# Kernel optimization log

Hardware: AMD Instinct MI355X
Metric: run time of the kernel (lower is better)

## Reference

```python
import jax, jax.numpy as jnp
import numpy as np
from jax import lax
from jax.scipy.special import logsumexp

B, T, K = 256, 1024, 64


def setup_inputs() -> dict:
    key = jax.random.key(0)
    k1, k2, k3 = jax.random.split(key, 3)
    y_true = jax.random.randint(k1, (B, T), 0, K)  # 0 == pad tag
    emissions = jax.random.normal(k2, (B, T, K), dtype=jnp.float32)
    transition = jax.random.normal(k3, (K, K), dtype=jnp.float32) * 0.1
    return {"y_true": y_true, "emissions": emissions, "transition": transition}


def _log_partition(emissions, mask, transition):
    # alpha_0 = emissions[:, 0, :] (TF code does not mask step 0)
    alpha0 = emissions[:, 0, :]  # [B, K]

    def step(alpha, xs):
        emit_t, m_t = xs  # [B, K], [B]
        # score[b, i, j] = alpha[b, i] + transition[i, j] + emit_t[b, j]
        score = alpha[:, :, None] + transition[None, :, :] + emit_t[:, None, :]
        new_a = logsumexp(score, axis=1)  # [B, K]
        new_a = jnp.where(m_t[:, None] > 0, new_a, alpha)
        return new_a, None

    xs = (jnp.swapaxes(emissions[:, 1:, :], 0, 1),  # [T-1, B, K]
          jnp.swapaxes(mask[:, 1:], 0, 1))           # [T-1, B]
    alpha, _ = lax.scan(step, alpha0, xs)
    return logsumexp(alpha, axis=1)  # [B]


def reference(y_true, emissions, transition):
    mask = (y_true != 0).astype(emissions.dtype)  # [B, T]
    yt = y_true.astype(jnp.int32)

    # emission scores of the gold path on masked emissions
    em_masked = emissions * mask[:, :, None]
    e_scores = jnp.take_along_axis(em_masked, yt[:, :, None], axis=2)[..., 0].sum(axis=1)  # [B]

    # transition scores of the gold path
    prev, nxt = yt[:, :-1], yt[:, 1:]
    t_scores = (transition[prev, nxt] * mask[:, 1:]).sum(axis=1)  # [B]

    log_z = _log_partition(emissions, mask, transition)  # [B]
    ll = e_scores + t_scores - log_z
    return -jnp.mean(ll)
```

## Files before the change

### kernel.cpp

```cpp
#include <hip/hip_runtime.h>

#define LOG2E 1.44269504088896340736f
#define LN2   0.69314718055994530942f

typedef short bf8 __attribute__((ext_vector_type(8)));
typedef float f4  __attribute__((ext_vector_type(4)));

static __device__ __forceinline__ unsigned short f2bf_rne(float f) {
    unsigned u = __float_as_uint(f);
    u += 0x7FFFu + ((u >> 16) & 1u);
    return (unsigned short)(u >> 16);
}
static __device__ __forceinline__ unsigned pack_bf_trunc(float lo, float hi) {
    return __builtin_amdgcn_perm(__float_as_uint(hi), __float_as_uint(lo), 0x07060302u);
}

__global__ __attribute__((amdgpu_flat_work_group_size(64, 64), amdgpu_waves_per_eu(1, 4)))
void crf_scan(const int* __restrict__ yg, const float* __restrict__ em,
              const float* __restrict__ tr, unsigned short* __restrict__ Pg)
{
    constexpr int T = 1024, STR = 72;
    const int c = blockIdx.x, b = blockIdx.y;
    const int lane = threadIdx.x, nl = lane & 15, q = lane >> 4;

    __shared__ __align__(16) unsigned short p_sh[64 * STR];
    __shared__ float d_sh[64];

    #pragma unroll
    for (int r = 0; r < 9; ++r) {
        uint4 z; z.x = z.y = z.z = z.w = 0u;
        *(uint4*)&p_sh[lane * STR + r * 8] = z;
    }
    p_sh[lane * STR + lane] = 0x3F80;

    bf8 afr[4][2];
    #pragma unroll
    for (int mt = 0; mt < 4; ++mt)
        #pragma unroll
        for (int kt = 0; kt < 2; ++kt) {
            bf8 v;
            #pragma unroll
            for (int j = 0; j < 8; ++j) {
                const int k = 32 * kt + 8 * q + j, m = 16 * mt + nl;
                v[j] = (short)f2bf_rne(exp2f(tr[k * 64 + m] * LOG2E));
            }
            afr[mt][kt] = v;
        }

    const int t0 = 1 + 64 * c;
    const int nsteps = (c == 15) ? 63 : 64;
    const float* emb = em + (size_t)b * T * 64;

    int tl = t0 + lane; if (tl > T - 1) tl = T - 1;
    const int yvl = yg[b * T + tl];
    const unsigned long long msk = __ballot(lane < nsteps && yvl != 0);

    float ldc = emb[t0 * 64 + lane];
    for (int s = 0; s < nsteps; ++s) {
        int tn = t0 + s + 1; if (tn > T - 1) tn = T - 1;
        const float ldn = emb[tn * 64 + lane];
        if ((msk >> s) & 1ull) {
            d_sh[lane] = exp2f(ldc * LOG2E - 7.0f);
            bf8 bfr[2][4];
            #pragma unroll
            for (int kt = 0; kt < 2; ++kt)
                #pragma unroll
                for (int nt = 0; nt < 4; ++nt)
                    bfr[kt][nt] = *(const bf8*)&p_sh[(16 * nt + nl) * STR + 32 * kt + 8 * q];
            float d16[4][4];
            #pragma unroll
            for (int mt = 0; mt < 4; ++mt)
                #pragma unroll
                for (int r = 0; r < 4; ++r)
                    d16[mt][r] = d_sh[16 * mt + 4 * q + r];
            #pragma unroll
            for (int mt = 0; mt < 4; ++mt)
                #pragma unroll
                for (int nt = 0; nt < 4; ++nt) {
                    f4 acc = __builtin_amdgcn_mfma_f32_16x16x32_bf16(
                                 afr[mt][0], bfr[0][nt], (f4)(0.0f), 0, 0, 0);
                    acc = __builtin_amdgcn_mfma_f32_16x16x32_bf16(
                                 afr[mt][1], bfr[1][nt], acc, 0, 0, 0);
                    const unsigned p0 = pack_bf_trunc(acc[0] * d16[mt][0], acc[1] * d16[mt][1]);
                    const unsigned p1 = pack_bf_trunc(acc[2] * d16[mt][2], acc[3] * d16[mt][3]);
                    uint2 w; w.x = p0; w.y = p1;
                    *(uint2*)&p_sh[(16 * nt + nl) * STR + 16 * mt + 4 * q] = w;
                }
        }
        ldc = ldn;
    }

    unsigned short* pg = Pg + ((size_t)(b * 16 + c) << 12);
    #pragma unroll
    for (int r = 0; r < 8; ++r)
        *(uint4*)(pg + lane * 64 + r * 8) = *(const uint4*)&p_sh[lane * STR + r * 8];
}

__global__ __attribute__((amdgpu_flat_work_group_size(64, 64), amdgpu_waves_per_eu(1, 1)))
void crf_combine(const int* __restrict__ yg, const float* __restrict__ em,
                 const float* __restrict__ tr, const unsigned short* __restrict__ Pg,
                 float* __restrict__ out)
{
    constexpr int T = 1024;
    const int b = blockIdx.x, j = threadIdx.x;
    __shared__ __align__(16) float v_sh[64];

    const float e0 = em[(size_t)b * T * 64 + j];
    float M0 = e0;
    #pragma unroll
    for (int o = 32; o > 0; o >>= 1) M0 = fmaxf(M0, __shfl_xor(M0, o, 64));
    float v = exp2f((e0 - M0) * LOG2E);
    float L = M0;

    const int* yb = yg + b * T;
    int cnt = 0; float ep = 0.f, tp = 0.f;
    for (int t = 1 + j; t < T; t += 64) {
        const int yt = yb[t];
        if (yt != 0) {
            ++cnt;
            tp += tr[yb[t - 1] * 64 + yt];
            ep += em[((size_t)b * T + t) * 64 + yt];
        }
    }
    if (j == 0) {
        const int y0 = yb[0];
        if (y0 != 0) ep += em[(size_t)b * T * 64 + y0];
    }

    const unsigned short* pgb = Pg + ((size_t)(b * 16) << 12);
    for (int c = 0; c < 16; ++c) {
        v_sh[j] = v;
        const unsigned short* row = pgb + ((size_t)c << 12) + j * 64;
        float s0 = 0.f, s1 = 0.f, s2 = 0.f, s3 = 0.f;
        #pragma unroll
        for (int r = 0; r < 8; ++r) {
            const uint4 qq = *(const uint4*)(row + r * 8);
            const float* vp = &v_sh[r * 8];
            s0 = fmaf(__uint_as_float(qq.x << 16),         vp[0], s0);
            s1 = fmaf(__uint_as_float(qq.x & 0xFFFF0000u), vp[1], s1);
            s2 = fmaf(__uint_as_float(qq.y << 16),         vp[2], s2);
            s3 = fmaf(__uint_as_float(qq.y & 0xFFFF0000u), vp[3], s3);
            s0 = fmaf(__uint_as_float(qq.z << 16),         vp[4], s0);
            s1 = fmaf(__uint_as_float(qq.z & 0xFFFF0000u), vp[5], s1);
            s2 = fmaf(__uint_as_float(qq.w << 16),         vp[6], s2);
            s3 = fmaf(__uint_as_float(qq.w & 0xFFFF0000u), vp[7], s3);
        }
        float s = (s0 + s1) + (s2 + s3);
        const unsigned sb = (unsigned)__builtin_amdgcn_readlane((int)__float_as_uint(s), 0);
        const int ef = (int)((sb >> 23) & 0xFF);
        if (ef > 0 && ef < 255 && ef != 127) {
            const int E = ef - 127;
            s *= __uint_as_float((unsigned)(127 - E) << 23);
            L += (float)E * LN2;
        }
        v = s;
    }

    float vs = v, eps = ep, tps = tp; int cs = cnt;
    #pragma unroll
    for (int o = 32; o > 0; o >>= 1) {
        vs  += __shfl_xor(vs, o, 64);
        eps += __shfl_xor(eps, o, 64);
        tps += __shfl_xor(tps, o, 64);
        cs  += __shfl_xor(cs, o, 64);
    }
    if (j == 0) {
        const float logz = L + 7.0f * LN2 * (float)cs + __log2f(vs) * LN2;
        const float ll = eps + tps - logz;
        atomicAdd(out, ll * (-1.0f / 256.0f));
    }
}

extern "C" void kernel_launch(void* const* d_in, const int* in_sizes, int n_in,
                              void* d_out, int out_size, void* d_ws, size_t ws_size,
                              hipStream_t stream) {
    const int*   y  = (const int*)d_in[0];
    const float* em = (const float*)d_in[1];
    const float* tr = (const float*)d_in[2];
    float* out = (float*)d_out;
    unsigned short* Pg = (unsigned short*)d_ws;

    hipMemsetAsync(out, 0, sizeof(float), stream);
    crf_scan<<<dim3(16, 256), dim3(64), 0, stream>>>(y, em, tr, Pg);
    crf_combine<<<dim3(256), dim3(64), 0, stream>>>(y, em, tr, Pg, out);
}
```

Before: 243.3 us.

## Keep chunk product matrix in registers via 16x16x16 MFMA and split combine work

The scan kernel no longer round-trips the running 64x64 product matrix through LDS each step. It uses 16x16x16 bf16 MFMA, whose output fragment layout matches the B operand layout, so results are fed back directly from registers. The combine kernel grows to four waves: one runs the chunk-serial matrix-vector chain with double-buffered global prefetch, and the other three compute the gold-path emission and transition scores in parallel. The changes trade more MFMA instructions (half-K shapes) and more register pressure for removing LDS traffic and barriers, and an inline-asm fallback with manual nops is added for toolchains that lack the builtin.

```diff
diff --git a/kernel.cpp b/kernel.cpp
--- a/kernel.cpp
+++ b/kernel.cpp
@@ -3,7 +3,7 @@
 #define LOG2E 1.44269504088896340736f
 #define LN2   0.69314718055994530942f
 
-typedef short bf8 __attribute__((ext_vector_type(8)));
+typedef short bf4 __attribute__((ext_vector_type(4)));
 typedef float f4  __attribute__((ext_vector_type(4)));
 
 static __device__ __forceinline__ unsigned short f2bf_rne(float f) {
@@ -15,36 +15,55 @@
     return __builtin_amdgcn_perm(__float_as_uint(hi), __float_as_uint(lo), 0x07060302u);
 }
 
-__global__ __attribute__((amdgpu_flat_work_group_size(64, 64), amdgpu_waves_per_eu(1, 4)))
+static __device__ __forceinline__ f4 mfma16(bf4 a, bf4 b, f4 c) {
+#if __has_builtin(__builtin_amdgcn_mfma_f32_16x16x16bf16_1k)
+    return __builtin_amdgcn_mfma_f32_16x16x16bf16_1k(a, b, c, 0, 0, 0);
+#else
+    f4 d;
+    asm("v_mfma_f32_16x16x16_bf16 %0, %1, %2, %3" : "=v"(d) : "v"(a), "v"(b), "v"(c));
+    return d;
+#endif
+}
+static __device__ __forceinline__ void mfma_fence() {
+#if !__has_builtin(__builtin_amdgcn_mfma_f32_16x16x16bf16_1k)
+    asm volatile("s_nop 7\ns_nop 7");
+#endif
+}
+
+__global__ __attribute__((amdgpu_flat_work_group_size(64, 64), amdgpu_waves_per_eu(4)))
 void crf_scan(const int* __restrict__ yg, const float* __restrict__ em,
               const float* __restrict__ tr, unsigned short* __restrict__ Pg)
 {
-    constexpr int T = 1024, STR = 72;
+    constexpr int T = 1024;
     const int c = blockIdx.x, b = blockIdx.y;
     const int lane = threadIdx.x, nl = lane & 15, q = lane >> 4;
 
-    __shared__ __align__(16) unsigned short p_sh[64 * STR];
-    __shared__ float d_sh[64];
-
-    #pragma unroll
-    for (int r = 0; r < 9; ++r) {
-        uint4 z; z.x = z.y = z.z = z.w = 0u;
-        *(uint4*)&p_sh[lane * STR + r * 8] = z;
-    }
-    p_sh[lane * STR + lane] = 0x3F80;
-
-    bf8 afr[4][2];
+    __shared__ __align__(16) float d_sh[64];
+
+    bf4 afr[4][4];
     #pragma unroll
     for (int mt = 0; mt < 4; ++mt)
         #pragma unroll
-        for (int kt = 0; kt < 2; ++kt) {
-            bf8 v;
-            #pragma unroll
-            for (int j = 0; j < 8; ++j) {
-                const int k = 32 * kt + 8 * q + j, m = 16 * mt + nl;
+        for (int kt = 0; kt < 4; ++kt) {
+            bf4 v;
+            #pragma unroll
+            for (int j = 0; j < 4; ++j) {
+                const int k = 16 * kt + 4 * q + j, m = 16 * mt + nl;
                 v[j] = (short)f2bf_rne(exp2f(tr[k * 64 + m] * LOG2E));
             }
             afr[mt][kt] = v;
+        }
+
+    bf4 bfr[4][4];
+    #pragma unroll
+    for (int kt = 0; kt < 4; ++kt)
+        #pragma unroll
+        for (int nt = 0; nt < 4; ++nt) {
+            bf4 v;
+            #pragma unroll
+            for (int j = 0; j < 4; ++j)
+                v[j] = (short)((kt == nt && nl == 4 * q + j) ? 0x3F80 : 0);
+            bfr[kt][nt] = v;
         }
 
     const int t0 = 1 + 64 * c;
@@ -61,113 +80,145 @@
         const float ldn = emb[tn * 64 + lane];
         if ((msk >> s) & 1ull) {
             d_sh[lane] = exp2f(ldc * LOG2E - 7.0f);
-            bf8 bfr[2][4];
-            #pragma unroll
-            for (int kt = 0; kt < 2; ++kt)
+            f4 dq[4];
+            #pragma unroll
+            for (int mt = 0; mt < 4; ++mt)
+                dq[mt] = *(const f4*)&d_sh[16 * mt + 4 * q];
+            #pragma unroll
+            for (int nt = 0; nt < 4; ++nt) {
+                f4 acc[4];
                 #pragma unroll
-                for (int nt = 0; nt < 4; ++nt)
-                    bfr[kt][nt] = *(const bf8*)&p_sh[(16 * nt + nl) * STR + 32 * kt + 8 * q];
-            float d16[4][4];
-            #pragma unroll
-            for (int mt = 0; mt < 4; ++mt)
+                for (int mt = 0; mt < 4; ++mt) {
+                    f4 a = mfma16(afr[mt][0], bfr[0][nt], (f4)(0.0f));
+                    a = mfma16(afr[mt][1], bfr[1][nt], a);
+                    a = mfma16(afr[mt][2], bfr[2][nt], a);
+                    a = mfma16(afr[mt][3], bfr[3][nt], a);
+                    acc[mt] = a;
+                }
+                mfma_fence();
                 #pragma unroll
-                for (int r = 0; r < 4; ++r)
-                    d16[mt][r] = d_sh[16 * mt + 4 * q + r];
-            #pragma unroll
-            for (int mt = 0; mt < 4; ++mt)
-                #pragma unroll
-                for (int nt = 0; nt < 4; ++nt) {
-                    f4 acc = __builtin_amdgcn_mfma_f32_16x16x32_bf16(
-                                 afr[mt][0], bfr[0][nt], (f4)(0.0f), 0, 0, 0);
-                    acc = __builtin_amdgcn_mfma_f32_16x16x32_bf16(
-                                 afr[mt][1], bfr[1][nt], acc, 0, 0, 0);
-                    const unsigned p0 = pack_bf_trunc(acc[0] * d16[mt][0], acc[1] * d16[mt][1]);
-                    const unsigned p1 = pack_bf_trunc(acc[2] * d16[mt][2], acc[3] * d16[mt][3]);
-                    uint2 w; w.x = p0; w.y = p1;
-                    *(uint2*)&p_sh[(16 * nt + nl) * STR + 16 * mt + 4 * q] = w;
+                for (int mt = 0; mt < 4; ++mt) {
+                    union { uint2 u; bf4 v2; } wv;
+                    wv.u.x = pack_bf_trunc(acc[mt][0] * dq[mt][0], acc[mt][1] * dq[mt][1]);
+                    wv.u.y = pack_bf_trunc(acc[mt][2] * dq[mt][2], acc[mt][3] * dq[mt][3]);
+                    bfr[mt][nt] = wv.v2;
                 }
+            }
         }
         ldc = ldn;
     }
 
     unsigned short* pg = Pg + ((size_t)(b * 16 + c) << 12);
     #pragma unroll
-    for (int r = 0; r < 8; ++r)
-        *(uint4*)(pg + lane * 64 + r * 8) = *(const uint4*)&p_sh[lane * STR + r * 8];
-}
-
-__global__ __attribute__((amdgpu_flat_work_group_size(64, 64), amdgpu_waves_per_eu(1, 1)))
+    for (int nt = 0; nt < 4; ++nt)
+        #pragma unroll
+        for (int kt = 0; kt < 4; ++kt)
+            *(uint2*)(pg + (16 * nt + nl) * 64 + 16 * kt + 4 * q) =
+                *(const uint2*)&bfr[kt][nt];
+}
+
+__global__ __attribute__((amdgpu_flat_work_group_size(256, 256)))
 void crf_combine(const int* __restrict__ yg, const float* __restrict__ em,
                  const float* __restrict__ tr, const unsigned short* __restrict__ Pg,
                  float* __restrict__ out)
 {
     constexpr int T = 1024;
-    const int b = blockIdx.x, j = threadIdx.x;
+    const int b = blockIdx.x, tid = threadIdx.x;
+    const int w = tid >> 6, j = tid & 63;
+
     __shared__ __align__(16) float v_sh[64];
-
-    const float e0 = em[(size_t)b * T * 64 + j];
-    float M0 = e0;
-    #pragma unroll
-    for (int o = 32; o > 0; o >>= 1) M0 = fmaxf(M0, __shfl_xor(M0, o, 64));
-    float v = exp2f((e0 - M0) * LOG2E);
-    float L = M0;
-
-    const int* yb = yg + b * T;
-    int cnt = 0; float ep = 0.f, tp = 0.f;
-    for (int t = 1 + j; t < T; t += 64) {
-        const int yt = yb[t];
-        if (yt != 0) {
-            ++cnt;
-            tp += tr[yb[t - 1] * 64 + yt];
-            ep += em[((size_t)b * T + t) * 64 + yt];
-        }
+    __shared__ float red[3][4];
+
+    float ep = 0.f, tp = 0.f; int cnt = 0;
+    float v = 0.f, L = 0.f, vs = 0.f;
+
+    if (w == 0) {
+        const float e0 = em[(size_t)b * T * 64 + j];
+        float M0 = e0;
+        #pragma unroll
+        for (int o = 32; o > 0; o >>= 1) M0 = fmaxf(M0, __shfl_xor(M0, o, 64));
+        v = exp2f((e0 - M0) * LOG2E);
+        L = M0;
+
+        const unsigned short* row = Pg + ((size_t)(b * 16) << 12) + j * 64;
+        uint4 pA[8], pB[8];
+        #pragma unroll
+        for (int r = 0; r < 8; ++r) pA[r] = *(const uint4*)(row + r * 8);
+
+#define CHUNK_STEP(CUR, NXT, CIDX)                                                 \
+        do {                                                                       \
+            if ((CIDX) + 1 < 16) {      \
+                const unsigned short* rn = row + ((size_t)((CIDX) + 1) << 12);     \
+                _Pragma("unroll")                                                  \
+                for (int r = 0; r < 8; ++r) NXT[r] = *(const uint4*)(rn + r * 8);  \
+            }                                                                      \
+            v_sh[j] = v;                             \
+            float s0 = 0.f, s1 = 0.f, s2 = 0.f, s3 = 0.f;                          \
+            _Pragma("unroll")                                                      \
+            for (int r = 0; r < 8; ++r) {                                          \
+                const uint4 qq = CUR[r];                                           \
+                const float* vp = &v_sh[r * 8];                                    \
+                s0 = fmaf(__uint_as_float(qq.x << 16),         vp[0], s0);         \
+                s1 = fmaf(__uint_as_float(qq.x & 0xFFFF0000u), vp[1], s1);         \
+                s2 = fmaf(__uint_as_float(qq.y << 16),         vp[2], s2);         \
+                s3 = fmaf(__uint_as_float(qq.y & 0xFFFF0000u), vp[3], s3);         \
+                s0 = fmaf(__uint_as_float(qq.z << 16),         vp[4], s0);         \
+                s1 = fmaf(__uint_as_float(qq.z & 0xFFFF0000u), vp[5], s1);         \
+                s2 = fmaf(__uint_as_float(qq.w << 16),         vp[6], s2);         \
+                s3 = fmaf(__uint_as_float(qq.w & 0xFFFF0000u), vp[7], s3);         \
+            }                                                                      \
+            float s = (s0 + s1) + (s2 + s3);                                       \
+            const unsigned sb =                                                    \
+                (unsigned)__builtin_amdgcn_readlane((int)__float_as_uint(s), 0);   \
+            const int ef = (int)((sb >> 23) & 0xFF);                               \
+            if (ef > 0 && ef < 255 && ef != 127) {       \
+                const int E = ef - 127;                                            \
+                s *= __uint_as_float((unsigned)(127 - E) << 23);                   \
+                L += (float)E * LN2;                                               \
+            }                                                                      \
+            v = s;                                                                 \
+        } while (0)
+
+        for (int cc = 0; cc < 16; cc += 2) {
+            CHUNK_STEP(pA, pB, cc);
+            CHUNK_STEP(pB, pA, cc + 1);
+        }
+#undef CHUNK_STEP
+
+        vs = v;
+        #pragma unroll
+        for (int o = 32; o > 0; o >>= 1) vs += __shfl_xor(vs, o, 64);
+    } else {
+        const int* yb = yg + b * T;
+        const int wt = tid - 64;
+        for (int t = 1 + wt; t < T; t += 192) {
+            const int yt = yb[t];
+            if (yt != 0) {
+                ++cnt;
+                tp += tr[yb[t - 1] * 64 + yt];
+                ep += em[((size_t)b * T + t) * 64 + yt];
+            }
+        }
+        if (tid == 64) {
+            const int y0 = yb[0];
+            if (y0 != 0) ep += em[(size_t)b * T * 64 + y0];
+        }
+        #pragma unroll
+        for (int o = 32; o > 0; o >>= 1) {
+            ep  += __shfl_xor(ep, o, 64);
+            tp  += __shfl_xor(tp, o, 64);
+            cnt += __shfl_xor(cnt, o, 64);
+        }
+        if (j == 0) { red[0][w] = ep; red[1][w] = tp; red[2][w] = (float)cnt; }
     }
-    if (j == 0) {
-        const int y0 = yb[0];
-        if (y0 != 0) ep += em[(size_t)b * T * 64 + y0];
-    }
-
-    const unsigned short* pgb = Pg + ((size_t)(b * 16) << 12);
-    for (int c = 0; c < 16; ++c) {
-        v_sh[j] = v;
-        const unsigned short* row = pgb + ((size_t)c << 12) + j * 64;
-        float s0 = 0.f, s1 = 0.f, s2 = 0.f, s3 = 0.f;
-        #pragma unroll
-        for (int r = 0; r < 8; ++r) {
-            const uint4 qq = *(const uint4*)(row + r * 8);
-            const float* vp = &v_sh[r * 8];
-            s0 = fmaf(__uint_as_float(qq.x << 16),         vp[0], s0);
-            s1 = fmaf(__uint_as_float(qq.x & 0xFFFF0000u), vp[1], s1);
-            s2 = fmaf(__uint_as_float(qq.y << 16),         vp[2], s2);
-            s3 = fmaf(__uint_as_float(qq.y & 0xFFFF0000u), vp[3], s3);
-            s0 = fmaf(__uint_as_float(qq.z << 16),         vp[4], s0);
-            s1 = fmaf(__uint_as_float(qq.z & 0xFFFF0000u), vp[5], s1);
-            s2 = fmaf(__uint_as_float(qq.w << 16),         vp[6], s2);
-            s3 = fmaf(__uint_as_float(qq.w & 0xFFFF0000u), vp[7], s3);
-        }
-        float s = (s0 + s1) + (s2 + s3);
-        const unsigned sb = (unsigned)__builtin_amdgcn_readlane((int)__float_as_uint(s), 0);
-        const int ef = (int)((sb >> 23) & 0xFF);
-        if (ef > 0 && ef < 255 && ef != 127) {
-            const int E = ef - 127;
-            s *= __uint_as_float((unsigned)(127 - E) << 23);
-            L += (float)E * LN2;
-        }
-        v = s;
-    }
-
-    float vs = v, eps = ep, tps = tp; int cs = cnt;
-    #pragma unroll
-    for (int o = 32; o > 0; o >>= 1) {
-        vs  += __shfl_xor(vs, o, 64);
-        eps += __shfl_xor(eps, o, 64);
-        tps += __shfl_xor(tps, o, 64);
-        cs  += __shfl_xor(cs, o, 64);
-    }
-    if (j == 0) {
-        const float logz = L + 7.0f * LN2 * (float)cs + __log2f(vs) * LN2;
-        const float ll = eps + tps - logz;
-        atomicAdd(out, ll * (-1.0f / 256.0f));
+    __syncthreads();
+
+    if (tid == 0) {
+        const float eps = red[0][1] + red[0][2] + red[0][3];
+        const float tps = red[1][1] + red[1][2] + red[1][3];
+        const float cs  = red[2][1] + red[2][2] + red[2][3];
+        const float logz = L + 7.0f * LN2 * cs + __log2f(vs) * LN2;
+        atomicAdd(out, (eps + tps - logz) * (-1.0f / 256.0f));
     }
 }
 
@@ -182,5 +233,5 @@
 
     hipMemsetAsync(out, 0, sizeof(float), stream);
     crf_scan<<<dim3(16, 256), dim3(64), 0, stream>>>(y, em, tr, Pg);
-    crf_combine<<<dim3(256), dim3(64), 0, stream>>>(y, em, tr, Pg, out);
-}
+    crf_combine<<<dim3(256), dim3(256), 0, stream>>>(y, em, tr, Pg, out);
+}
```

Result: no change. 246.2 us (+1.2%).
